# Optimization experiments

Hardware: AMD Instinct MI355X
Metric: run time of the kernel (lower is better)

The kernel has to match this reference:

```python
import jax, jax.numpy as jnp
import numpy as np

B, N, D, H = 2, 2048, 1024, 16
DH = D // H  # head dim = 64


def setup_inputs() -> dict:
    key = jax.random.key(0)
    k1, k2, k3 = jax.random.split(key, 3)
    x = jax.random.normal(k1, (B, N, D), dtype=jnp.float32)
    # per-head Linear(D, 3*DH): stacked weights (H, D, 3*DH), biases (H, 3*DH)
    W_qkv = jax.random.normal(k2, (H, D, 3 * DH), dtype=jnp.float32) * 0.02
    b_qkv = jnp.zeros((H, 3 * DH), dtype=jnp.float32)
    W_proj = jax.random.normal(k3, (D, D), dtype=jnp.float32) * 0.02
    b_proj = jnp.zeros((D,), dtype=jnp.float32)
    return {"x": x, "W_qkv": W_qkv, "b_qkv": b_qkv, "W_proj": W_proj, "b_proj": b_proj}


def reference(x, W_qkv, b_qkv, W_proj, b_proj):
    b, n, d = x.shape
    h = W_qkv.shape[0]
    dh = W_qkv.shape[2] // 3
    # all heads' kqv projections at once: (B, H, N, 3*DH)
    qkv = jnp.einsum('bnd,hde->bhne', x, W_qkv) + b_qkv[None, :, None, :]
    # original chunks in order k, q, v
    k, q, v = jnp.split(qkv, 3, axis=-1)  # each (B, H, N, DH)
    # scores[b,h,n,m] = q_n . k_m / sqrt(dh)
    scores = jnp.einsum('bhnd,bhmd->bhnm', q, k) / jnp.sqrt(jnp.asarray(dh, x.dtype))
    causal = jnp.tril(jnp.ones((n, n), dtype=bool))
    scores = jnp.where(causal[None, None, :, :], scores, -jnp.inf)
    A = jax.nn.softmax(scores, axis=-1)
    out = jnp.einsum('bhnm,bhmd->bhnd', A, v)
    # concat heads (head-major order matches the torch cat over head list)
    out = out.transpose(0, 2, 1, 3).reshape(b, n, h * dh)
    return out @ W_proj + b_proj
```

## Files before the change

kernel.cpp:

```cpp
#include <hip/hip_runtime.h>
#include <hip/hip_bf16.h>

typedef __hip_bfloat16 HBF;
typedef __bf16 bf16x8 __attribute__((ext_vector_type(8)));
typedef __bf16 bf16x4 __attribute__((ext_vector_type(4)));
typedef float f32x4 __attribute__((ext_vector_type(4)));
typedef float float4v __attribute__((ext_vector_type(4)));

__device__ __forceinline__ float toF(float x) { return x; }
__device__ __forceinline__ float toF(HBF x) { return __bfloat162float(x); }

#define MFMA16(a, b, c) __builtin_amdgcn_mfma_f32_16x16x32_bf16((a), (b), (c), 0, 0, 0)
#define EXP2F(x) __builtin_amdgcn_exp2f(x)
#define QSCALE 0.18033688011112042f
#define MEMFENCE asm volatile("" ::: "memory")

__device__ __forceinline__ void gload_lds16(const HBF* g, HBF* l) {
  __builtin_amdgcn_global_load_lds((const __attribute__((address_space(1))) void*)g,
                                   (__attribute__((address_space(3))) void*)l, 16, 0, 0);
}

__global__ void prep_k(const float* __restrict__ x, HBF* __restrict__ xb,
                       const float* __restrict__ Wqkv, HBF* __restrict__ wqkv_t,
                       const float* __restrict__ Wproj, HBF* __restrict__ wproj_t) {
  const int bid = blockIdx.x, tid = threadIdx.x;
  if (bid < 4096) {
    int i = bid * 256 + tid;
    float4v a = reinterpret_cast<const float4v*>(x)[i];
    HBF o[4] = {__float2bfloat16(a.x), __float2bfloat16(a.y),
                __float2bfloat16(a.z), __float2bfloat16(a.w)};
    *reinterpret_cast<ulonglong1*>(&xb[i * 4]) = *reinterpret_cast<ulonglong1*>(o);
    return;
  }
  __shared__ float tile[32][33];
  const float* in;
  HBF* out;
  int R, C, gx, gy;
  size_t base;
  if (bid < 7168) {
    int t = bid - 4096;
    int gz = t / 192, rem = t % 192;
    gy = rem / 6; gx = rem % 6;
    R = 1024; C = 192;
    base = (size_t)gz * R * C;
    in = Wqkv; out = wqkv_t;
  } else {
    int t = bid - 7168;
    gy = t / 32; gx = t % 32;
    R = 1024; C = 1024;
    base = 0;
    in = Wproj; out = wproj_t;
  }
  int r0 = gy * 32, c0 = gx * 32;
  int tx = tid & 31, ty = tid >> 5;
#pragma unroll
  for (int i = ty; i < 32; i += 8)
    tile[i][tx] = in[base + (size_t)(r0 + i) * C + c0 + tx];
  __syncthreads();
#pragma unroll
  for (int i = ty; i < 32; i += 8)
    out[base + (size_t)(c0 + i) * R + r0 + tx] = __float2bfloat16(tile[tx][i]);
}

__launch_bounds__(512, 1)
__global__ void gemm_qkv_8ph(const HBF* __restrict__ A, const HBF* __restrict__ Bt,
                             const float* __restrict__ bias,
                             HBF* __restrict__ Kout, HBF* __restrict__ Qout,
                             HBF* __restrict__ Vtout) {
  __shared__ __align__(16) HBF As[2][16384];
  __shared__ __align__(16) HBF Bs[2][12288];
  const int tid = threadIdx.x, lane = tid & 63, w = tid >> 6;
  const int lo = lane & 15, g4 = lane >> 4;
  const int wr = w >> 2, wc = w & 3;
  const int s = ((int)blockIdx.x & 7) * 32 + ((int)blockIdx.x >> 3);
  const int bx = s & 15, by = s >> 4;
  const int m0 = by * 256, n0 = bx * 192;
  const int NT = 16;

  f32x4 acc[8][3];
#pragma unroll
  for (int i = 0; i < 8; i++)
#pragma unroll
    for (int j = 0; j < 3; j++) acc[i][j] = (f32x4){0.f, 0.f, 0.f, 0.f};
  bf16x8 af[8][2], bfr[3][2];

  const int rl0 = w * 8 + (lane >> 3);
  const int rl1 = 64 + rl0;
  const int kc0 = (lane & 7) ^ (rl0 & 7);
  const int kc1 = (lane & 7) ^ (rl1 & 7);

  auto stageA = [&](int kt, int hf) {
    HBF* base = &As[kt & 1][hf * 8192];
    const int r0g = m0 + hf * 128;
    gload_lds16(A + (size_t)(r0g + rl0) * 1024 + kt * 64 + kc0 * 8, base + w * 512);
    gload_lds16(A + (size_t)(r0g + rl1) * 1024 + kt * 64 + kc1 * 8, base + 4096 + w * 512);
  };
  auto stageB = [&](int kt, int g) {
    gload_lds16(Bt + (size_t)(n0 + g * 64 + rl0) * 1024 + kt * 64 + kc0 * 8,
                &Bs[kt & 1][g * 4096] + w * 512);
  };
  auto ldA = [&](int bb, int mt, int ks) -> bf16x8 {
    int row = wr * 128 + mt * 16 + lo;
    return *reinterpret_cast<const bf16x8*>(&As[bb][row * 64 + ((ks * 32 + g4 * 8) ^ ((row & 7) * 8))]);
  };
  auto ldB = [&](int bb, int nt, int ks) -> bf16x8 {
    int row = wc * 48 + nt * 16 + lo;
    return *reinterpret_cast<const bf16x8*>(&Bs[bb][row * 64 + ((ks * 32 + g4 * 8) ^ ((row & 7) * 8))]);
  };

  stageA(0, 0); stageA(0, 1); stageB(0, 0); stageB(0, 1); stageB(0, 2);
  stageA(1, 0); stageA(1, 1);
  asm volatile("s_waitcnt vmcnt(4)" ::: "memory");
  __builtin_amdgcn_s_barrier();
  MEMFENCE;

  for (int t = 0; t < NT; ++t) {
    const int bb = t & 1;
#pragma unroll
    for (int mt = 0; mt < 4; ++mt) { af[mt][0] = ldA(bb, mt, 0); af[mt][1] = ldA(bb, mt, 1); }
#pragma unroll
    for (int nt = 0; nt < 2; ++nt) { bfr[nt][0] = ldB(bb, nt, 0); bfr[nt][1] = ldB(bb, nt, 1); }
    if (t + 1 < NT) stageB(t + 1, 0);
    MEMFENCE; __builtin_amdgcn_s_barrier(); MEMFENCE;
    __builtin_amdgcn_s_setprio(1);
#pragma unroll
    for (int mt = 0; mt < 4; ++mt)
#pragma unroll
      for (int nt = 0; nt < 2; ++nt)
#pragma unroll
        for (int ks = 0; ks < 2; ++ks) acc[mt][nt] = MFMA16(af[mt][ks], bfr[nt][ks], acc[mt][nt]);
    __builtin_amdgcn_s_setprio(0);
    MEMFENCE; __builtin_amdgcn_s_barrier(); MEMFENCE;
#pragma unroll
    for (int mt = 4; mt < 8; ++mt) { af[mt][0] = ldA(bb, mt, 0); af[mt][1] = ldA(bb, mt, 1); }
    if (t + 1 < NT) { stageB(t + 1, 1); stageB(t + 1, 2); }
    MEMFENCE; __builtin_amdgcn_s_barrier(); MEMFENCE;
    __builtin_amdgcn_s_setprio(1);
#pragma unroll
    for (int mt = 4; mt < 8; ++mt)
#pragma unroll
      for (int nt = 0; nt < 2; ++nt)
#pragma unroll
        for (int ks = 0; ks < 2; ++ks) acc[mt][nt] = MFMA16(af[mt][ks], bfr[nt][ks], acc[mt][nt]);
    __builtin_amdgcn_s_setprio(0);
    MEMFENCE; __builtin_amdgcn_s_barrier(); MEMFENCE;
    bfr[2][0] = ldB(bb, 2, 0); bfr[2][1] = ldB(bb, 2, 1);
    if (t + 2 < NT) stageA(t + 2, 0);
    MEMFENCE; __builtin_amdgcn_s_barrier(); MEMFENCE;
    __builtin_amdgcn_s_setprio(1);
#pragma unroll
    for (int mt = 0; mt < 4; ++mt)
#pragma unroll
      for (int ks = 0; ks < 2; ++ks) acc[mt][2] = MFMA16(af[mt][ks], bfr[2][ks], acc[mt][2]);
    __builtin_amdgcn_s_setprio(0);
    MEMFENCE; __builtin_amdgcn_s_barrier(); MEMFENCE;
    if (t + 2 < NT) stageA(t + 2, 1);
    MEMFENCE; __builtin_amdgcn_s_barrier(); MEMFENCE;
    __builtin_amdgcn_s_setprio(1);
#pragma unroll
    for (int mt = 4; mt < 8; ++mt)
#pragma unroll
      for (int ks = 0; ks < 2; ++ks) acc[mt][2] = MFMA16(af[mt][ks], bfr[2][ks], acc[mt][2]);
    __builtin_amdgcn_s_setprio(0);
    asm volatile("s_waitcnt vmcnt(4)" ::: "memory");
    __builtin_amdgcn_s_barrier();
    MEMFENCE;
  }

#pragma unroll
  for (int mt = 0; mt < 8; ++mt) {
    int mrow = m0 + wr * 128 + mt * 16 + g4 * 4;
#pragma unroll
    for (int nt = 0; nt < 3; ++nt) {
      int e = wc * 48 + nt * 16 + lo;
      float bv = bias[bx * 192 + e];
#pragma unroll
      for (int r = 0; r < 4; ++r) {
        int mm = mrow + r;
        int b = mm >> 11, n = mm & 2047;
        float v = acc[mt][nt][r] + bv;
        size_t bh64 = (size_t)(b * 16 + bx);
        if (e < 64)       Kout[(bh64 * 2048 + n) * 64 + e] = __float2bfloat16(v);
        else if (e < 128) Qout[(bh64 * 2048 + n) * 64 + e - 64] = __float2bfloat16(v * QSCALE);
        else              Vtout[(bh64 * 64 + (e - 128)) * 2048 + n] = __float2bfloat16(v);
      }
    }
  }
}

__launch_bounds__(256)
__global__ void gemm_proj_k(const HBF* __restrict__ A, const HBF* __restrict__ Bt,
                            int M, int N, int K, const float* __restrict__ bias,
                            float* __restrict__ Cout) {
  __shared__ __align__(16) HBF As[128 * 64];
  __shared__ __align__(16) HBF Bs[128 * 64];
  const int tid = threadIdx.x;
  const int lane = tid & 63;
  const int w = tid >> 6;
  const int lo = lane & 15, g4 = lane >> 4;
  const int m0 = blockIdx.y * 128, n0 = blockIdx.x * 128;
  const int wr = w >> 1, wc = w & 1;

  const f32x4 zero = {0.f, 0.f, 0.f, 0.f};
  f32x4 acc[4][4];
#pragma unroll
  for (int i = 0; i < 4; i++)
#pragma unroll
    for (int j = 0; j < 4; j++) acc[i][j] = zero;

  for (int k0 = 0; k0 < K; k0 += 64) {
#pragma unroll
    for (int c = 0; c < 4; ++c) {
      int chunk = c * 256 + tid;
      int row = chunk >> 3, kc = (chunk & 7) * 8;
      HBF* ldsA = As + (size_t)(c * 256 + w * 64) * 8;
      HBF* ldsB = Bs + (size_t)(c * 256 + w * 64) * 8;
      gload_lds16(A + (size_t)(m0 + row) * K + k0 + kc, ldsA);
      gload_lds16(Bt + (size_t)(n0 + row) * K + k0 + kc, ldsB);
    }
    __syncthreads();
#pragma unroll
    for (int kk = 0; kk < 2; ++kk) {
      bf16x8 af[4], bfr[4];
#pragma unroll
      for (int i = 0; i < 4; i++)
        af[i] = *reinterpret_cast<const bf16x8*>(As + (size_t)(wr * 64 + i * 16 + lo) * 64 + kk * 32 + g4 * 8);
#pragma unroll
      for (int j = 0; j < 4; j++)
        bfr[j] = *reinterpret_cast<const bf16x8*>(Bs + (size_t)(wc * 64 + j * 16 + lo) * 64 + kk * 32 + g4 * 8);
#pragma unroll
      for (int i = 0; i < 4; i++)
#pragma unroll
        for (int j = 0; j < 4; j++) acc[i][j] = MFMA16(af[i], bfr[j], acc[i][j]);
    }
    __syncthreads();
  }

#pragma unroll
  for (int i = 0; i < 4; i++) {
    int mrow = m0 + wr * 64 + i * 16 + g4 * 4;
#pragma unroll
    for (int j = 0; j < 4; j++) {
      int col = n0 + wc * 64 + j * 16 + lo;
      float bv = bias[col];
#pragma unroll
      for (int r = 0; r < 4; r++)
        Cout[(size_t)(mrow + r) * N + col] = acc[i][j][r] + bv;
    }
  }
}

__launch_bounds__(256)
__global__ void attn_fwd_k(const HBF* __restrict__ Qb, const HBF* __restrict__ Kb,
                           const HBF* __restrict__ Vt, HBF* __restrict__ Ob) {
  __shared__ __align__(16) HBF Ks[2][64 * 64];
  __shared__ __align__(16) HBF Vs[2][64 * 64];
  __shared__ __align__(16) HBF pLds[4][16 * 64];
  const int tid = threadIdx.x;
  const int lane = tid & 63;
  const int w = tid >> 6;
  const int lo = lane & 15, g4 = lane >> 4;

  const int lin = blockIdx.x;
  const int xcd = lin & 7, c = lin >> 3;
  const int cu = c & 31, r4 = c >> 5;
  const int bh = xcd * 4 + r4;
  const int j = (r4 == 1 || r4 == 2) ? 31 - cu : cu;
  const int b = bh >> 4, h = bh & 15;
  const int qrow0 = j * 64 + w * 16;
  const int nkv = j + 1;

  const HBF* Qp = Qb + (size_t)bh * 2048 * 64;
  const HBF* Kp = Kb + (size_t)bh * 2048 * 64;
  const HBF* Vp = Vt + (size_t)bh * 64 * 2048;

  bf16x8 qf[2];
#pragma unroll
  for (int ds = 0; ds < 2; ds++)
    qf[ds] = *reinterpret_cast<const bf16x8*>(Qp + (size_t)(qrow0 + lo) * 64 + ds * 32 + g4 * 8);

  const f32x4 zero = {0.f, 0.f, 0.f, 0.f};
  f32x4 o[4];
  float m = -1e30f, l = 0.f;
#pragma unroll
  for (int j4 = 0; j4 < 4; j4++) o[j4] = zero;

  const int srow = (lane >> 3) & 7;
  const int sch = lane & 7;
  const int psw = (lo & 7) << 4;

  auto stage = [&](int kv0, int sb) {
#pragma unroll
    for (int cc = 0; cc < 2; cc++) {
      int seg = w * 2 + cc;
      int row = seg * 8 + srow;
      gload_lds16(Kp + (size_t)(kv0 + row) * 64 + ((sch ^ (row & 7)) * 8), &Ks[sb][seg * 512]);
      gload_lds16(Vp + (size_t)row * 2048 + kv0 + ((sch ^ (row & 7)) * 8), &Vs[sb][seg * 512]);
    }
  };

  stage(0, 0);
  __syncthreads();

  for (int t = 0; t < nkv; ++t) {
    const int kv0 = t * 64;
    const int sb = t & 1;
    if (t + 1 < nkv) stage(kv0 + 64, sb ^ 1);

    f32x4 st[4];
#pragma unroll
    for (int kt = 0; kt < 4; kt++) {
      int krow = kt * 16 + lo;
      bf16x8 kf0 = *reinterpret_cast<const bf16x8*>(&Ks[sb][krow * 64 + ((g4 ^ (krow & 7)) * 8)]);
      bf16x8 kf1 = *reinterpret_cast<const bf16x8*>(&Ks[sb][krow * 64 + (((4 + g4) ^ (krow & 7)) * 8)]);
      f32x4 z = zero;
      z = MFMA16(kf0, qf[0], z);
      z = MFMA16(kf1, qf[1], z);
      st[kt] = z;
    }

    const int q = qrow0 + lo;
    float pmax = -1e30f;
    if (t == nkv - 1) {
#pragma unroll
      for (int kt = 0; kt < 4; kt++)
#pragma unroll
        for (int r = 0; r < 4; r++) {
          int key = kv0 + kt * 16 + g4 * 4 + r;
          float v = (key <= q) ? st[kt][r] : -1e30f;
          st[kt][r] = v;
          pmax = fmaxf(pmax, v);
        }
    } else {
#pragma unroll
      for (int kt = 0; kt < 4; kt++)
#pragma unroll
        for (int r = 0; r < 4; r++) pmax = fmaxf(pmax, st[kt][r]);
    }
    pmax = fmaxf(pmax, __shfl_xor(pmax, 16));
    pmax = fmaxf(pmax, __shfl_xor(pmax, 32));
    if (__any(pmax > m + 11.5f)) {
      float mn = fmaxf(m, pmax);
      float al = EXP2F(m - mn);
      m = mn;
      l *= al;
      float alr[4];
#pragma unroll
      for (int r = 0; r < 4; r++) alr[r] = __shfl(al, g4 * 4 + r);
#pragma unroll
      for (int j4 = 0; j4 < 4; j4++)
#pragma unroll
        for (int r = 0; r < 4; r++) o[j4][r] *= alr[r];
    }
#pragma unroll
    for (int kt = 0; kt < 4; kt++)
#pragma unroll
      for (int r = 0; r < 4; r++) {
        float p = EXP2F(st[kt][r] - m);
        st[kt][r] = p;
        l += p;
      }
#pragma unroll
    for (int kt = 0; kt < 4; kt++) {
      bf16x4 pk;
#pragma unroll
      for (int r = 0; r < 4; r++) pk[r] = (__bf16)st[kt][r];
      *reinterpret_cast<bf16x4*>(&pLds[w][lo * 64 + (((kt * 32 + g4 * 8) ^ psw) >> 1)]) = pk;
    }
    asm volatile("s_waitcnt lgkmcnt(0)" ::: "memory");
    __builtin_amdgcn_sched_barrier(0);

    bf16x8 pa[2];
#pragma unroll
    for (int ks = 0; ks < 2; ks++)
      pa[ks] = *reinterpret_cast<const bf16x8*>(&pLds[w][lo * 64 + (((ks * 64 + g4 * 16) ^ psw) >> 1)]);
#pragma unroll
    for (int j4 = 0; j4 < 4; j4++) {
      int vrow = j4 * 16 + lo;
#pragma unroll
      for (int ks = 0; ks < 2; ks++) {
        bf16x8 vb = *reinterpret_cast<const bf16x8*>(&Vs[sb][vrow * 64 + (((ks * 4 + g4) ^ (vrow & 7)) * 8)]);
        o[j4] = MFMA16(pa[ks], vb, o[j4]);
      }
    }
    __syncthreads();
  }

  l += __shfl_xor(l, 16);
  l += __shfl_xor(l, 32);
  float linv = 1.f / l;
  float lr[4];
#pragma unroll
  for (int r = 0; r < 4; r++) lr[r] = __shfl(linv, g4 * 4 + r);
#pragma unroll
  for (int j4 = 0; j4 < 4; j4++)
#pragma unroll
    for (int r = 0; r < 4; r++) {
      int q = qrow0 + g4 * 4 + r;
      Ob[(size_t)(b * 2048 + q) * 1024 + h * 64 + j4 * 16 + lo] =
          __float2bfloat16(o[j4][r] * lr[r]);
    }
}

extern "C" void kernel_launch(void* const* d_in, const int* in_sizes, int n_in,
                              void* d_out, int out_size, void* d_ws, size_t ws_size,
                              hipStream_t stream) {
  const float* x      = (const float*)d_in[0];
  const float* W_qkv  = (const float*)d_in[1];
  const float* b_qkv  = (const float*)d_in[2];
  const float* W_proj = (const float*)d_in[3];
  const float* b_proj = (const float*)d_in[4];
  float* out = (float*)d_out;

  const int B = 2, N = 2048, D = 1024, H = 16, DH = 64;
  const int M = B * N;

  char* ws = (char*)d_ws;
  HBF* xb      = (HBF*)ws; ws += (size_t)M * D * 2;
  HBF* wqkv_t  = (HBF*)ws; ws += (size_t)H * 3 * DH * D * 2;
  HBF* wproj_t = (HBF*)ws; ws += (size_t)D * D * 2;
  HBF* Qb      = (HBF*)ws; ws += (size_t)B * H * N * DH * 2;
  HBF* Kb      = (HBF*)ws; ws += (size_t)B * H * N * DH * 2;
  HBF* Vt      = (HBF*)ws; ws += (size_t)B * H * DH * N * 2;
  HBF* Ob      = (HBF*)ws; ws += (size_t)M * D * 2;

  prep_k<<<8192, 256, 0, stream>>>(x, xb, W_qkv, wqkv_t, W_proj, wproj_t);
  gemm_qkv_8ph<<<256, 512, 0, stream>>>(xb, wqkv_t, b_qkv, Kb, Qb, Vt);
  attn_fwd_k<<<1024, 256, 0, stream>>>(Qb, Kb, Vt, Ob);
  gemm_proj_k<<<dim3(D / 128, M / 128), 256, 0, stream>>>(Ob, wproj_t, M, D, D, b_proj, out);
}
```

Baseline: 121.1 us.

## Pair short and long causal query strips per block for balanced attention work

```diff
diff --git a/kernel.cpp b/kernel.cpp
--- a/kernel.cpp
+++ b/kernel.cpp
@@ -250,7 +250,7 @@
   }
 }
 
-__launch_bounds__(256)
+__launch_bounds__(256, 4)
 __global__ void attn_fwd_k(const HBF* __restrict__ Qb, const HBF* __restrict__ Kb,
                            const HBF* __restrict__ Vt, HBF* __restrict__ Ob) {
   __shared__ __align__(16) HBF Ks[2][64 * 64];
@@ -263,27 +263,30 @@
 
   const int lin = blockIdx.x;
   const int xcd = lin & 7, c = lin >> 3;
-  const int cu = c & 31, r4 = c >> 5;
-  const int bh = xcd * 4 + r4;
-  const int j = (r4 == 1 || r4 == 2) ? 31 - cu : cu;
+  const int bh = xcd * 4 + (c >> 5);
+  const int i = c & 31;
   const int b = bh >> 4, h = bh & 15;
-  const int qrow0 = j * 64 + w * 16;
-  const int nkv = j + 1;
+  const int qA16 = i * 32 + (w & 1) * 16;
+  const int qB16 = (63 - i) * 32 + (w >> 1) * 16;
+  const int nkvA = i / 2 + 1;
+  const int nkvB = (63 - i) / 2 + 1;
 
   const HBF* Qp = Qb + (size_t)bh * 2048 * 64;
   const HBF* Kp = Kb + (size_t)bh * 2048 * 64;
   const HBF* Vp = Vt + (size_t)bh * 64 * 2048;
 
-  bf16x8 qf[2];
-#pragma unroll
-  for (int ds = 0; ds < 2; ds++)
-    qf[ds] = *reinterpret_cast<const bf16x8*>(Qp + (size_t)(qrow0 + lo) * 64 + ds * 32 + g4 * 8);
+  bf16x8 qfA[2], qfB[2];
+#pragma unroll
+  for (int ds = 0; ds < 2; ds++) {
+    qfA[ds] = *reinterpret_cast<const bf16x8*>(Qp + (size_t)(qA16 + lo) * 64 + ds * 32 + g4 * 8);
+    qfB[ds] = *reinterpret_cast<const bf16x8*>(Qp + (size_t)(qB16 + lo) * 64 + ds * 32 + g4 * 8);
+  }
 
   const f32x4 zero = {0.f, 0.f, 0.f, 0.f};
-  f32x4 o[4];
-  float m = -1e30f, l = 0.f;
-#pragma unroll
-  for (int j4 = 0; j4 < 4; j4++) o[j4] = zero;
+  f32x4 oA[4], oB[4];
+  float mA = -1e30f, lA = 0.f, mB = -1e30f, lB = 0.f;
+#pragma unroll
+  for (int j4 = 0; j4 < 4; j4++) { oA[j4] = zero; oB[j4] = zero; }
 
   const int srow = (lane >> 3) & 7;
   const int sch = lane & 7;
@@ -299,14 +302,8 @@
     }
   };
 
-  stage(0, 0);
-  __syncthreads();
-
-  for (int t = 0; t < nkv; ++t) {
-    const int kv0 = t * 64;
-    const int sb = t & 1;
-    if (t + 1 < nkv) stage(kv0 + 64, sb ^ 1);
-
+  auto proc = [&](int kv0, int sb, const bf16x8 (&qf)[2], f32x4 (&o)[4],
+                  float& m, float& l, int qb16, bool diag) {
     f32x4 st[4];
 #pragma unroll
     for (int kt = 0; kt < 4; kt++) {
@@ -318,10 +315,9 @@
       z = MFMA16(kf1, qf[1], z);
       st[kt] = z;
     }
-
-    const int q = qrow0 + lo;
+    const int q = qb16 + lo;
     float pmax = -1e30f;
-    if (t == nkv - 1) {
+    if (diag) {
 #pragma unroll
       for (int kt = 0; kt < 4; kt++)
 #pragma unroll
@@ -369,7 +365,6 @@
     }
     asm volatile("s_waitcnt lgkmcnt(0)" ::: "memory");
     __builtin_amdgcn_sched_barrier(0);
-
     bf16x8 pa[2];
 #pragma unroll
     for (int ks = 0; ks < 2; ks++)
@@ -383,22 +378,39 @@
         o[j4] = MFMA16(pa[ks], vb, o[j4]);
       }
     }
+  };
+
+  stage(0, 0);
+  __syncthreads();
+
+  for (int t = 0; t < nkvB; ++t) {
+    const int kv0 = t * 64;
+    const int sb = t & 1;
+    if (t + 1 < nkvB) stage(kv0 + 64, sb ^ 1);
+    proc(kv0, sb, qfB, oB, mB, lB, qB16, t == nkvB - 1);
+    if (t < nkvA) proc(kv0, sb, qfA, oA, mA, lA, qA16, t == nkvA - 1);
     __syncthreads();
   }
 
-  l += __shfl_xor(l, 16);
-  l += __shfl_xor(l, 32);
-  float linv = 1.f / l;
-  float lr[4];
-#pragma unroll
-  for (int r = 0; r < 4; r++) lr[r] = __shfl(linv, g4 * 4 + r);
+  lB += __shfl_xor(lB, 16); lB += __shfl_xor(lB, 32);
+  lA += __shfl_xor(lA, 16); lA += __shfl_xor(lA, 32);
+  float liB = 1.f / lB, liA = 1.f / lA;
+  float lrB[4], lrA[4];
+#pragma unroll
+  for (int r = 0; r < 4; r++) {
+    lrB[r] = __shfl(liB, g4 * 4 + r);
+    lrA[r] = __shfl(liA, g4 * 4 + r);
+  }
 #pragma unroll
   for (int j4 = 0; j4 < 4; j4++)
 #pragma unroll
     for (int r = 0; r < 4; r++) {
-      int q = qrow0 + g4 * 4 + r;
-      Ob[(size_t)(b * 2048 + q) * 1024 + h * 64 + j4 * 16 + lo] =
-          __float2bfloat16(o[j4][r] * lr[r]);
+      int qB = qB16 + g4 * 4 + r;
+      Ob[(size_t)(b * 2048 + qB) * 1024 + h * 64 + j4 * 16 + lo] =
+          __float2bfloat16(oB[j4][r] * lrB[r]);
+      int qA = qA16 + g4 * 4 + r;
+      Ob[(size_t)(b * 2048 + qA) * 1024 + h * 64 + j4 * 16 + lo] =
+          __float2bfloat16(oA[j4][r] * lrA[r]);
     }
 }
 
```

Measured after the change: 136.0 us. +12.3%, slower.

## Process 128-key KV tiles per iteration and schedule attention blocks heaviest-first

Applied to the files above, without the earlier changes.

```diff
diff --git a/kernel.cpp b/kernel.cpp
--- a/kernel.cpp
+++ b/kernel.cpp
@@ -250,12 +250,12 @@
   }
 }
 
-__launch_bounds__(256)
+__launch_bounds__(256, 2)
 __global__ void attn_fwd_k(const HBF* __restrict__ Qb, const HBF* __restrict__ Kb,
                            const HBF* __restrict__ Vt, HBF* __restrict__ Ob) {
-  __shared__ __align__(16) HBF Ks[2][64 * 64];
-  __shared__ __align__(16) HBF Vs[2][64 * 64];
-  __shared__ __align__(16) HBF pLds[4][16 * 64];
+  __shared__ __align__(16) HBF Ks[2][2][4096];
+  __shared__ __align__(16) HBF Vs[2][2][4096];
+  __shared__ __align__(16) HBF pLds[4][2048];
   const int tid = threadIdx.x;
   const int lane = tid & 63;
   const int w = tid >> 6;
@@ -263,12 +263,11 @@
 
   const int lin = blockIdx.x;
   const int xcd = lin & 7, c = lin >> 3;
-  const int cu = c & 31, r4 = c >> 5;
-  const int bh = xcd * 4 + r4;
-  const int j = (r4 == 1 || r4 == 2) ? 31 - cu : cu;
+  const int bh = xcd * 4 + (c & 3);
+  const int j = 31 - (c >> 2);
   const int b = bh >> 4, h = bh & 15;
   const int qrow0 = j * 64 + w * 16;
-  const int nkv = j + 1;
+  const int nkv = (j + 2) >> 1;
 
   const HBF* Qp = Qb + (size_t)bh * 2048 * 64;
   const HBF* Kp = Kb + (size_t)bh * 2048 * 64;
@@ -291,51 +290,61 @@
 
   auto stage = [&](int kv0, int sb) {
 #pragma unroll
-    for (int cc = 0; cc < 2; cc++) {
-      int seg = w * 2 + cc;
-      int row = seg * 8 + srow;
-      gload_lds16(Kp + (size_t)(kv0 + row) * 64 + ((sch ^ (row & 7)) * 8), &Ks[sb][seg * 512]);
-      gload_lds16(Vp + (size_t)row * 2048 + kv0 + ((sch ^ (row & 7)) * 8), &Vs[sb][seg * 512]);
-    }
+    for (int sub = 0; sub < 2; sub++)
+#pragma unroll
+      for (int cc = 0; cc < 2; cc++) {
+        int seg = w * 2 + cc;
+        int row = seg * 8 + srow;
+        gload_lds16(Kp + (size_t)(kv0 + sub * 64 + row) * 64 + ((sch ^ (row & 7)) * 8),
+                    &Ks[sb][sub][seg * 512]);
+        gload_lds16(Vp + (size_t)row * 2048 + kv0 + sub * 64 + ((sch ^ (row & 7)) * 8),
+                    &Vs[sb][sub][seg * 512]);
+      }
   };
 
   stage(0, 0);
   __syncthreads();
 
   for (int t = 0; t < nkv; ++t) {
-    const int kv0 = t * 64;
+    const int kv0 = t * 128;
     const int sb = t & 1;
-    if (t + 1 < nkv) stage(kv0 + 64, sb ^ 1);
-
-    f32x4 st[4];
-#pragma unroll
-    for (int kt = 0; kt < 4; kt++) {
-      int krow = kt * 16 + lo;
-      bf16x8 kf0 = *reinterpret_cast<const bf16x8*>(&Ks[sb][krow * 64 + ((g4 ^ (krow & 7)) * 8)]);
-      bf16x8 kf1 = *reinterpret_cast<const bf16x8*>(&Ks[sb][krow * 64 + (((4 + g4) ^ (krow & 7)) * 8)]);
-      f32x4 z = zero;
-      z = MFMA16(kf0, qf[0], z);
-      z = MFMA16(kf1, qf[1], z);
-      st[kt] = z;
-    }
+    if (t + 1 < nkv) stage(kv0 + 128, sb ^ 1);
+
+    f32x4 st[2][4];
+#pragma unroll
+    for (int sub = 0; sub < 2; sub++)
+#pragma unroll
+      for (int kt = 0; kt < 4; kt++) {
+        int krow = kt * 16 + lo;
+        bf16x8 kf0 = *reinterpret_cast<const bf16x8*>(&Ks[sb][sub][krow * 64 + ((g4 ^ (krow & 7)) * 8)]);
+        bf16x8 kf1 = *reinterpret_cast<const bf16x8*>(&Ks[sb][sub][krow * 64 + (((4 + g4) ^ (krow & 7)) * 8)]);
+        f32x4 z = zero;
+        z = MFMA16(kf0, qf[0], z);
+        z = MFMA16(kf1, qf[1], z);
+        st[sub][kt] = z;
+      }
 
     const int q = qrow0 + lo;
     float pmax = -1e30f;
     if (t == nkv - 1) {
 #pragma unroll
-      for (int kt = 0; kt < 4; kt++)
-#pragma unroll
-        for (int r = 0; r < 4; r++) {
-          int key = kv0 + kt * 16 + g4 * 4 + r;
-          float v = (key <= q) ? st[kt][r] : -1e30f;
-          st[kt][r] = v;
-          pmax = fmaxf(pmax, v);
-        }
+      for (int sub = 0; sub < 2; sub++)
+#pragma unroll
+        for (int kt = 0; kt < 4; kt++)
+#pragma unroll
+          for (int r = 0; r < 4; r++) {
+            int key = kv0 + sub * 64 + kt * 16 + g4 * 4 + r;
+            float v = (key <= q) ? st[sub][kt][r] : -1e30f;
+            st[sub][kt][r] = v;
+            pmax = fmaxf(pmax, v);
+          }
     } else {
 #pragma unroll
-      for (int kt = 0; kt < 4; kt++)
-#pragma unroll
-        for (int r = 0; r < 4; r++) pmax = fmaxf(pmax, st[kt][r]);
+      for (int sub = 0; sub < 2; sub++)
+#pragma unroll
+        for (int kt = 0; kt < 4; kt++)
+#pragma unroll
+          for (int r = 0; r < 4; r++) pmax = fmaxf(pmax, st[sub][kt][r]);
     }
     pmax = fmaxf(pmax, __shfl_xor(pmax, 16));
     pmax = fmaxf(pmax, __shfl_xor(pmax, 32));
@@ -353,33 +362,40 @@
         for (int r = 0; r < 4; r++) o[j4][r] *= alr[r];
     }
 #pragma unroll
-    for (int kt = 0; kt < 4; kt++)
-#pragma unroll
-      for (int r = 0; r < 4; r++) {
-        float p = EXP2F(st[kt][r] - m);
-        st[kt][r] = p;
-        l += p;
+    for (int sub = 0; sub < 2; sub++)
+#pragma unroll
+      for (int kt = 0; kt < 4; kt++)
+#pragma unroll
+        for (int r = 0; r < 4; r++) {
+          float p = EXP2F(st[sub][kt][r] - m);
+          st[sub][kt][r] = p;
+          l += p;
+        }
+#pragma unroll
+    for (int sub = 0; sub < 2; sub++)
+#pragma unroll
+      for (int kt = 0; kt < 4; kt++) {
+        bf16x4 pk;
+#pragma unroll
+        for (int r = 0; r < 4; r++) pk[r] = (__bf16)st[sub][kt][r];
+        *reinterpret_cast<bf16x4*>(
+            &pLds[w][lo * 128 + (((sub * 128 + kt * 32 + g4 * 8) ^ psw) >> 1)]) = pk;
       }
-#pragma unroll
-    for (int kt = 0; kt < 4; kt++) {
-      bf16x4 pk;
-#pragma unroll
-      for (int r = 0; r < 4; r++) pk[r] = (__bf16)st[kt][r];
-      *reinterpret_cast<bf16x4*>(&pLds[w][lo * 64 + (((kt * 32 + g4 * 8) ^ psw) >> 1)]) = pk;
-    }
     asm volatile("s_waitcnt lgkmcnt(0)" ::: "memory");
     __builtin_amdgcn_sched_barrier(0);
 
-    bf16x8 pa[2];
-#pragma unroll
-    for (int ks = 0; ks < 2; ks++)
-      pa[ks] = *reinterpret_cast<const bf16x8*>(&pLds[w][lo * 64 + (((ks * 64 + g4 * 16) ^ psw) >> 1)]);
+    bf16x8 pa[4];
+#pragma unroll
+    for (int ks = 0; ks < 4; ks++)
+      pa[ks] = *reinterpret_cast<const bf16x8*>(
+          &pLds[w][lo * 128 + (((ks * 64 + g4 * 16) ^ psw) >> 1)]);
 #pragma unroll
     for (int j4 = 0; j4 < 4; j4++) {
       int vrow = j4 * 16 + lo;
 #pragma unroll
-      for (int ks = 0; ks < 2; ks++) {
-        bf16x8 vb = *reinterpret_cast<const bf16x8*>(&Vs[sb][vrow * 64 + (((ks * 4 + g4) ^ (vrow & 7)) * 8)]);
+      for (int ks = 0; ks < 4; ks++) {
+        bf16x8 vb = *reinterpret_cast<const bf16x8*>(
+            &Vs[sb][ks >> 1][vrow * 64 + ((((ks & 1) * 4 + g4) ^ (vrow & 7)) * 8)]);
         o[j4] = MFMA16(pa[ks], vb, o[j4]);
       }
     }
```

Measured after the change: 111.8 us. 7.7% less time.
